# Kernel optimization log

Measured on AMD Instinct MI355X. Metric: run time of the kernel, lower is better.

## Reference

```python
import jax, jax.numpy as jnp
import numpy as np

N = 400000  # flattened batch*frames; each row holds 2 chains x 4 joints x 4x4 transforms


def _fk_chain(pose):
    # pose: [N, 2, 4, 4, 4] -> end-effector FK transform [N, 2, 4, 4]
    # fk = I @ P0 @ P1 @ P2 @ P3 (identity init is a no-op, kept implicitly)
    fk = pose[:, :, 0]
    for j in range(1, 4):
        fk = jnp.matmul(fk, pose[:, :, j])
    return fk


def setup_inputs() -> dict:
    key = jax.random.key(0)
    k1, k2, k3, k4 = jax.random.split(key, 4)
    return {
        "output_pose": jax.random.normal(k1, (N, 128), dtype=jnp.float32),
        "gt_pose": jax.random.normal(k2, (N, 128), dtype=jnp.float32),
        "gt_prev_pose": jax.random.normal(k3, (N, 128), dtype=jnp.float32),
        "gt_pos": jax.random.normal(k4, (N, 6), dtype=jnp.float32),
    }


def reference(output_pose, gt_pose, gt_prev_pose, gt_pos):
    out_p = output_pose.reshape(-1, 2, 4, 4, 4)
    gt_p = gt_pose.reshape(-1, 2, 4, 4, 4)
    gt_prev_p = gt_prev_pose.reshape(-1, 2, 4, 4, 4)

    output_fk = _fk_chain(out_p)[:, :, :3, 3]   # [N, 2, 3] end-effector positions
    gt_fk = _fk_chain(gt_p)[:, :, :3, 3]
    gt_prev_fk = _fk_chain(gt_prev_p)[:, :, :3, 3]

    gt_vel = gt_fk - gt_prev_fk
    output_vel = output_fk - gt_prev_fk

    pos_loss = jnp.mean((output_fk - gt_fk) ** 2)
    vel_loss = jnp.mean((output_vel - gt_vel) ** 2)
    return (pos_loss, vel_loss)
```

## Files before the change

kernel.cpp:

```cpp
#include <hip/hip_runtime.h>


#define N_CHAINS 800000
#define ITERS 4
#define BLOCK 256
#define BLOCKS (N_CHAINS * 4 / ITERS / BLOCK)
#define CHAIN_STRIDE (N_CHAINS / ITERS)
#define MEAN_DIV (400000.0 * 2.0 * 3.0)

template <int I>
__device__ __forceinline__ float qb(float x) {
    return __builtin_bit_cast(float,
        __builtin_amdgcn_mov_dpp(__builtin_bit_cast(int, x),
                                 I | (I << 2) | (I << 4) | (I << 6),
                                 0xF, 0xF, true));
}

__device__ __forceinline__ float fk_elem(float4 m0, float4 m1, float4 m2, float4 m3) {
    float v = m3.w;
    float v0, v1, v2, v3;
    v0 = qb<0>(v); v1 = qb<1>(v); v2 = qb<2>(v); v3 = qb<3>(v);
    v = m2.x * v0 + m2.y * v1 + m2.z * v2 + m2.w * v3;
    v0 = qb<0>(v); v1 = qb<1>(v); v2 = qb<2>(v); v3 = qb<3>(v);
    v = m1.x * v0 + m1.y * v1 + m1.z * v2 + m1.w * v3;
    v0 = qb<0>(v); v1 = qb<1>(v); v2 = qb<2>(v); v3 = qb<3>(v);
    v = m0.x * v0 + m0.y * v1 + m0.z * v2 + m0.w * v3;
    return v;
}

__global__ __launch_bounds__(BLOCK) void fk_loss_kernel(const float4* __restrict__ o4,
                                                        const float4* __restrict__ g4,
                                                        float* __restrict__ partial) {
    const int tid = blockIdx.x * BLOCK + threadIdx.x;
    const int k = tid & 3;
    const int q = tid >> 2;

    const float4* po = o4 + (size_t)q * 16 + k;
    const float4* pg = g4 + (size_t)q * 16 + k;
    float4 o0 = po[0], o1 = po[4], o2 = po[8], o3 = po[12];
    float4 g0 = pg[0], g1 = pg[4], g2 = pg[8], g3 = pg[12];

    float ss = 0.0f;
#pragma unroll
    for (int it = 0; it < ITERS; ++it) {
        float4 no0, no1, no2, no3, ng0, ng1, ng2, ng3;
        if (it + 1 < ITERS) {
            const size_t off = ((size_t)q + (size_t)(it + 1) * CHAIN_STRIDE) * 16 + k;
            const float4* qo = o4 + off;
            const float4* qg = g4 + off;
            no0 = qo[0]; no1 = qo[4]; no2 = qo[8]; no3 = qo[12];
            ng0 = qg[0]; ng1 = qg[4]; ng2 = qg[8]; ng3 = qg[12];
        }
        float fo = fk_elem(o0, o1, o2, o3);
        float fg = fk_elem(g0, g1, g2, g3);
        float d = fo - fg;
        ss += (k < 3) ? d * d : 0.0f;
        o0 = no0; o1 = no1; o2 = no2; o3 = no3;
        g0 = ng0; g1 = ng1; g2 = ng2; g3 = ng3;
    }

#pragma unroll
    for (int off = 32; off > 0; off >>= 1) ss += __shfl_down(ss, off, 64);
    __shared__ float part[BLOCK / 64];
    if ((threadIdx.x & 63) == 0) part[threadIdx.x >> 6] = ss;
    __syncthreads();
    if (threadIdx.x == 0)
        partial[blockIdx.x] = part[0] + part[1] + part[2] + part[3];
}

__global__ __launch_bounds__(BLOCK) void fk_finalize(const float* __restrict__ partial,
                                                     float* __restrict__ out) {
    double s = 0.0;
    for (int i = threadIdx.x; i < BLOCKS; i += BLOCK) s += (double)partial[i];
    __shared__ double dpart[BLOCK / 64];
#pragma unroll
    for (int off = 32; off > 0; off >>= 1) s += __shfl_down(s, off, 64);
    if ((threadIdx.x & 63) == 0) dpart[threadIdx.x >> 6] = s;
    __syncthreads();
    if (threadIdx.x == 0) {
        double b = dpart[0] + dpart[1] + dpart[2] + dpart[3];
        float v = (float)(b / MEAN_DIV);
        out[0] = v;
        out[1] = v;
    }
}

extern "C" void kernel_launch(void* const* d_in, const int* in_sizes, int n_in,
                              void* d_out, int out_size, void* d_ws, size_t ws_size,
                              hipStream_t stream) {
    const float4* output_pose = (const float4*)d_in[0];
    const float4* gt_pose     = (const float4*)d_in[1];
    float* out = (float*)d_out;
    float* partial = (float*)d_ws;

    fk_loss_kernel<<<BLOCKS, BLOCK, 0, stream>>>(output_pose, gt_pose, partial);
    fk_finalize<<<1, BLOCK, 0, stream>>>(partial, out);
}
```

Baseline: 76.01 us.

## Stage chain tiles through LDS with coalesced per-wave loads and persistent loop

Each wave now loads contiguous 256-float4 tiles with fully coalesced float4 accesses, writes them to per-wave LDS, and reads the strided matrix elements back from LDS for the DPP-based FK product. The grid shrinks to 1250 blocks with each wave looping over 10 tiles with register prefetch of the next tile. This targets the uncoalesced strided global loads of the previous layout. In exchange it adds LDS traffic, possible bank conflicts, and lower parallelism from fewer blocks. It also relies on no cross-lane sync within a wave for the LDS reuse.

```diff
diff --git a/kernel.cpp b/kernel.cpp
--- a/kernel.cpp
+++ b/kernel.cpp
@@ -2,10 +2,9 @@
 
 
 #define N_CHAINS 800000
-#define ITERS 4
 #define BLOCK 256
-#define BLOCKS (N_CHAINS * 4 / ITERS / BLOCK)
-#define CHAIN_STRIDE (N_CHAINS / ITERS)
+#define BLOCKS 1250
+#define ITERS 10
 #define MEAN_DIV (400000.0 * 2.0 * 3.0)
 
 template <int I>
@@ -28,40 +27,58 @@
     return v;
 }
 
-__global__ __launch_bounds__(BLOCK) void fk_loss_kernel(const float4* __restrict__ o4,
-                                                        const float4* __restrict__ g4,
-                                                        float* __restrict__ partial) {
-    const int tid = blockIdx.x * BLOCK + threadIdx.x;
-    const int k = tid & 3;
-    const int q = tid >> 2;
+__global__ __launch_bounds__(BLOCK, 5) void fk_loss_kernel(const float4* __restrict__ o4,
+                                                           const float4* __restrict__ g4,
+                                                           float* __restrict__ partial) {
+    __shared__ float4 lds[4][2][256];
+    const int wid  = threadIdx.x >> 6;
+    const int lane = threadIdx.x & 63;
+    const int q = lane >> 2;
+    const int k = lane & 3;
+    const int w = blockIdx.x * 4 + wid;
 
-    const float4* po = o4 + (size_t)q * 16 + k;
-    const float4* pg = g4 + (size_t)q * 16 + k;
-    float4 o0 = po[0], o1 = po[4], o2 = po[8], o3 = po[12];
-    float4 g0 = pg[0], g1 = pg[4], g2 = pg[8], g3 = pg[12];
+    float4* Lo = lds[wid][0];
+    float4* Lg = lds[wid][1];
+    const size_t wbase = (size_t)w * (ITERS * 256);
+
+    float4 nx[8];
+#pragma unroll
+    for (int t = 0; t < 4; ++t) nx[t]     = o4[wbase + t * 64 + lane];
+#pragma unroll
+    for (int t = 0; t < 4; ++t) nx[4 + t] = g4[wbase + t * 64 + lane];
+#pragma unroll
+    for (int t = 0; t < 4; ++t) Lo[t * 64 + lane] = nx[t];
+#pragma unroll
+    for (int t = 0; t < 4; ++t) Lg[t * 64 + lane] = nx[4 + t];
 
     float ss = 0.0f;
+#pragma unroll 1
+    for (int it = 0; it < ITERS; ++it) {
+        if (it + 1 < ITERS) {
+            const size_t b = wbase + (size_t)(it + 1) * 256;
 #pragma unroll
-    for (int it = 0; it < ITERS; ++it) {
-        float4 no0, no1, no2, no3, ng0, ng1, ng2, ng3;
+            for (int t = 0; t < 4; ++t) nx[t]     = o4[b + t * 64 + lane];
+#pragma unroll
+            for (int t = 0; t < 4; ++t) nx[4 + t] = g4[b + t * 64 + lane];
+        }
+        const int ib = q * 16 + k;
+        float4 mo0 = Lo[ib], mo1 = Lo[ib + 4], mo2 = Lo[ib + 8], mo3 = Lo[ib + 12];
+        float4 mg0 = Lg[ib], mg1 = Lg[ib + 4], mg2 = Lg[ib + 8], mg3 = Lg[ib + 12];
+        float fo = fk_elem(mo0, mo1, mo2, mo3);
+        float fg = fk_elem(mg0, mg1, mg2, mg3);
+        float d = fo - fg;
+        if (k < 3) ss += d * d;
         if (it + 1 < ITERS) {
-            const size_t off = ((size_t)q + (size_t)(it + 1) * CHAIN_STRIDE) * 16 + k;
-            const float4* qo = o4 + off;
-            const float4* qg = g4 + off;
-            no0 = qo[0]; no1 = qo[4]; no2 = qo[8]; no3 = qo[12];
-            ng0 = qg[0]; ng1 = qg[4]; ng2 = qg[8]; ng3 = qg[12];
+#pragma unroll
+            for (int t = 0; t < 4; ++t) Lo[t * 64 + lane] = nx[t];
+#pragma unroll
+            for (int t = 0; t < 4; ++t) Lg[t * 64 + lane] = nx[4 + t];
         }
-        float fo = fk_elem(o0, o1, o2, o3);
-        float fg = fk_elem(g0, g1, g2, g3);
-        float d = fo - fg;
-        ss += (k < 3) ? d * d : 0.0f;
-        o0 = no0; o1 = no1; o2 = no2; o3 = no3;
-        g0 = ng0; g1 = ng1; g2 = ng2; g3 = ng3;
     }
 
 #pragma unroll
     for (int off = 32; off > 0; off >>= 1) ss += __shfl_down(ss, off, 64);
-    __shared__ float part[BLOCK / 64];
+    __shared__ float part[4];
     if ((threadIdx.x & 63) == 0) part[threadIdx.x >> 6] = ss;
     __syncthreads();
     if (threadIdx.x == 0)
@@ -72,7 +89,7 @@
                                                      float* __restrict__ out) {
     double s = 0.0;
     for (int i = threadIdx.x; i < BLOCKS; i += BLOCK) s += (double)partial[i];
-    __shared__ double dpart[BLOCK / 64];
+    __shared__ double dpart[4];
 #pragma unroll
     for (int off = 32; off > 0; off >>= 1) s += __shfl_down(s, off, 64);
     if ((threadIdx.x & 63) == 0) dpart[threadIdx.x >> 6] = s;
```

Result: slower. 164.7 us (+116.7%).
